# Optimization experiments

Hardware: AMD Instinct MI355X
Metric: run time of the kernel (lower is better)

## Reference

```python
import jax, jax.numpy as jnp
import numpy as np

N = 100000   # nodes
C = 128      # in_channels
K = 32       # n_super_nodes
B = 64       # graphs (num segments)


def setup_inputs() -> dict:
    key = jax.random.key(0)
    k_x, k_b, k_w1, k_b1, k_w2, k_b2 = jax.random.split(key, 6)
    x = jax.random.normal(k_x, (N, C), dtype=jnp.float32)
    batch = jnp.sort(jax.random.randint(k_b, (N,), 0, B))
    # assign_mlp params: Linear(C,C) -> ReLU -> Linear(C,K); stored as [in,out]
    W1 = jax.random.normal(k_w1, (C, C), dtype=jnp.float32) / np.sqrt(C)
    b1 = jax.random.normal(k_b1, (C,), dtype=jnp.float32) * 0.01
    W2 = jax.random.normal(k_w2, (C, K), dtype=jnp.float32) / np.sqrt(C)
    b2 = jax.random.normal(k_b2, (K,), dtype=jnp.float32) * 0.01
    return {"x": x, "batch": batch, "W1": W1, "b1": b1, "W2": W2, "b2": b2}


def reference(x, batch, W1, b1, W2, b2):
    # assignment logits: MLP over node features
    h = jax.nn.relu(x @ W1 + b1)          # [N, C]
    s = jax.nn.softmax(h @ W2 + b2, axis=-1)  # [N, K]
    # outer product per node, then scatter-sum by graph id
    x_expanded = x[:, None, :] * s[:, :, None]  # [N, K, C]
    out = jax.ops.segment_sum(x_expanded, batch, num_segments=B)  # [B, K, C]
    return (out, s)
```

## Files before the change

### kernel.cpp

```cpp
#include <hip/hip_runtime.h>
#include <hip/hip_bf16.h>

#define NN 100000
#define CC 128
#define KK 32
#define BB 64

typedef __bf16 bf16x8 __attribute__((ext_vector_type(8)));
typedef float  f32x4  __attribute__((ext_vector_type(4)));

__device__ __forceinline__ unsigned short f2bf(float v) {
    union { float f; unsigned u; } a; a.f = v;
    unsigned r = a.u + 0x7FFF + ((a.u >> 16) & 1);
    return (unsigned short)(r >> 16);
}
__device__ __forceinline__ float bf2f(unsigned short h) {
    union { unsigned u; float f; } a; a.u = ((unsigned)h) << 16;
    return a.f;
}
__device__ __forceinline__ void unpack_hilo(uint4 a, uint4 b,
                                            bf16x8& hi8, bf16x8& lo8) {
    union { uint4 v[2]; unsigned short s[16]; } U;
    U.v[0] = a; U.v[1] = b;
    union { unsigned short s[8]; bf16x8 v; } H, L;
    #pragma unroll
    for (int j = 0; j < 8; ++j) { H.s[j] = U.s[2 * j]; L.s[j] = U.s[2 * j + 1]; }
    hi8 = H.v; lo8 = L.v;
}

__global__ __launch_bounds__(256) void hp_prep(const int* __restrict__ batch,
                                               const float* __restrict__ W1,
                                               const float* __restrict__ W2,
                                               int* __restrict__ bounds,
                                               unsigned short* __restrict__ w1f,
                                               unsigned short* __restrict__ w2f) {
    if (blockIdx.x == 0 && threadIdx.x <= BB) {
        const int b = threadIdx.x;
        int lo = 0, hi = NN;
        while (lo < hi) {
            const int mid = (lo + hi) >> 1;
            if (batch[mid] < b) lo = mid + 1; else hi = mid;
        }
        bounds[b] = lo;
    }
    const int t = blockIdx.x * 256 + threadIdx.x;
    for (int idx = t; idx < 16384; idx += 2048) {
        const int j    = idx & 7;
        const int lane = (idx >> 3) & 63;
        const int nt   = (idx >> 9) & 7;
        const int kt   = idx >> 12;
        const int k = kt * 32 + (lane >> 4) * 8 + j;
        const int n = nt * 16 + (lane & 15);
        const float w = W1[k * CC + n];
        const unsigned short h = f2bf(w);
        w1f[idx]         = h;
        w1f[16384 + idx] = f2bf(w - bf2f(h));
    }
    for (int idx = t; idx < 4096; idx += 2048) {
        const int j    = idx & 7;
        const int lane = (idx >> 3) & 63;
        const int nt   = (idx >> 9) & 1;
        const int kt   = idx >> 10;
        const int k = kt * 32 + (lane >> 4) * 8 + j;
        const int n = nt * 16 + (lane & 15);
        const float w = W2[k * KK + n];
        const unsigned short h = f2bf(w);
        w2f[idx]        = h;
        w2f[4096 + idx] = f2bf(w - bf2f(h));
    }
}

__global__ __launch_bounds__(256, 6) void hp_mlp(
    const float* __restrict__ x,
    const unsigned short* __restrict__ w1f,
    const unsigned short* __restrict__ w2f,
    const float* __restrict__ b1,
    const float* __restrict__ b2,
    float* __restrict__ s_out)
{
    __shared__ __align__(16) char uni[16896];
    __shared__ float lgT[32][36];
    __shared__ float redm[4][32];
    __shared__ float reds[4][32];

    unsigned short* xa   = (unsigned short*)uni;
    unsigned int*   hs16 = (unsigned int*)uni;

    const int t    = threadIdx.x;
    const int wave = __builtin_amdgcn_readfirstlane(t >> 6);
    const int lane = t & 63;
    const int base = blockIdx.x * 32;

    #pragma unroll
    for (int mt = 0; mt < 2; ++mt) {
        const int q  = mt * 4 + wave;
        const int n  = base + mt * 16 + (lane & 15);
        const int ck = wave * 32 + (lane >> 4) * 8;
        const float4 va = *(const float4*)(x + (size_t)n * CC + ck);
        const float4 vb = *(const float4*)(x + (size_t)n * CC + ck + 4);
        const float v[8] = {va.x, va.y, va.z, va.w, vb.x, vb.y, vb.z, vb.w};
        unsigned short hi[8], lo[8];
        #pragma unroll
        for (int j = 0; j < 8; ++j) {
            hi[j] = f2bf(v[j]);
            lo[j] = f2bf(v[j] - bf2f(hi[j]));
        }
        unsigned short* d0 = xa + (q * 64 + lane) * 8;
        unsigned short* d1 = d0 + 4096;
        *(ushort4*)(d0)     = make_ushort4(hi[0], hi[1], hi[2], hi[3]);
        *(ushort4*)(d0 + 4) = make_ushort4(hi[4], hi[5], hi[6], hi[7]);
        *(ushort4*)(d1)     = make_ushort4(lo[0], lo[1], lo[2], lo[3]);
        *(ushort4*)(d1 + 4) = make_ushort4(lo[4], lo[5], lo[6], lo[7]);
    }
    __syncthreads();

    f32x4 acc[2][2];
    #pragma unroll
    for (int mt = 0; mt < 2; ++mt)
        #pragma unroll
        for (int nl = 0; nl < 2; ++nl)
            acc[mt][nl] = (f32x4){0.f, 0.f, 0.f, 0.f};

    #pragma unroll
    for (int kt = 0; kt < 4; ++kt) {
        bf16x8 ah[2], al[2];
        #pragma unroll
        for (int mt = 0; mt < 2; ++mt) {
            ah[mt] = *(const bf16x8*)(xa + ((mt * 4 + kt) * 64 + lane) * 8);
            al[mt] = *(const bf16x8*)(xa + 4096 + ((mt * 4 + kt) * 64 + lane) * 8);
        }
        #pragma unroll
        for (int nl = 0; nl < 2; ++nl) {
            const int nt = 2 * wave + nl;
            const bf16x8 wh = *(const bf16x8*)(w1f + ((kt * 8 + nt) * 64 + lane) * 8);
            const bf16x8 wl = *(const bf16x8*)(w1f + 16384 + ((kt * 8 + nt) * 64 + lane) * 8);
            #pragma unroll
            for (int mt = 0; mt < 2; ++mt) {
                acc[mt][nl] = __builtin_amdgcn_mfma_f32_16x16x32_bf16(ah[mt], wh, acc[mt][nl], 0, 0, 0);
                acc[mt][nl] = __builtin_amdgcn_mfma_f32_16x16x32_bf16(al[mt], wh, acc[mt][nl], 0, 0, 0);
                acc[mt][nl] = __builtin_amdgcn_mfma_f32_16x16x32_bf16(ah[mt], wl, acc[mt][nl], 0, 0, 0);
            }
        }
    }
    __syncthreads();

    #pragma unroll
    for (int nl = 0; nl < 2; ++nl) {
        const int c = (2 * wave + nl) * 16 + (lane & 15);
        const float bv = b1[c];
        #pragma unroll
        for (int mt = 0; mt < 2; ++mt)
            #pragma unroll
            for (int r = 0; r < 4; ++r) {
                const int node = mt * 16 + (lane >> 4) * 4 + r;
                const float h = fmaxf(acc[mt][nl][r] + bv, 0.f);
                const unsigned short hi = f2bf(h);
                const unsigned short lo = f2bf(h - bf2f(hi));
                hs16[node * 132 + c] = (unsigned)hi | ((unsigned)lo << 16);
            }
    }
    __syncthreads();

    {
        const int mt2 = wave & 1, nt2 = wave >> 1;
        f32x4 dacc = (f32x4){0.f, 0.f, 0.f, 0.f};
        #pragma unroll
        for (int kt = 0; kt < 4; ++kt) {
            const unsigned* hp = hs16 + (mt2 * 16 + (lane & 15)) * 132
                                      + kt * 32 + (lane >> 4) * 8;
            const uint4 u0 = *(const uint4*)hp;
            const uint4 u1 = *(const uint4*)(hp + 4);
            bf16x8 ah, al;
            unpack_hilo(u0, u1, ah, al);
            const bf16x8 wh = *(const bf16x8*)(w2f + ((kt * 2 + nt2) * 64 + lane) * 8);
            const bf16x8 wl = *(const bf16x8*)(w2f + 4096 + ((kt * 2 + nt2) * 64 + lane) * 8);
            dacc = __builtin_amdgcn_mfma_f32_16x16x32_bf16(ah, wh, dacc, 0, 0, 0);
            dacc = __builtin_amdgcn_mfma_f32_16x16x32_bf16(al, wh, dacc, 0, 0, 0);
            dacc = __builtin_amdgcn_mfma_f32_16x16x32_bf16(ah, wl, dacc, 0, 0, 0);
        }
        const int kcol = nt2 * 16 + (lane & 15);
        #pragma unroll
        for (int r = 0; r < 4; ++r) {
            const int node = mt2 * 16 + (lane >> 4) * 4 + r;
            lgT[node][kcol] = dacc[r];
        }
    }
    __syncthreads();

    const int node = lane & 31;
    const int koff = ((lane >> 5) << 4) + wave * 4;
    const float4 bv2 = *(const float4*)(b2 + koff);
    const float4 lv  = *(const float4*)&lgT[node][koff];
    float lg[4] = {lv.x + bv2.x, lv.y + bv2.y, lv.z + bv2.z, lv.w + bv2.w};

    float m = fmaxf(fmaxf(lg[0], lg[1]), fmaxf(lg[2], lg[3]));
    m = fmaxf(m, __shfl_xor(m, 32));
    if (lane < 32) redm[wave][lane] = m;
    __syncthreads();
    const float M = fmaxf(fmaxf(redm[0][node], redm[1][node]),
                          fmaxf(redm[2][node], redm[3][node]));
    const float e0 = __expf(lg[0] - M);
    const float e1 = __expf(lg[1] - M);
    const float e2 = __expf(lg[2] - M);
    const float e3 = __expf(lg[3] - M);
    float sp = (e0 + e1) + (e2 + e3);
    sp += __shfl_xor(sp, 32);
    if (lane < 32) reds[wave][lane] = sp;
    __syncthreads();
    const float S = (reds[0][node] + reds[1][node]) + (reds[2][node] + reds[3][node]);
    const float inv = 1.f / S;
    *(float4*)(s_out + (size_t)(base + node) * KK + koff) =
        make_float4(e0 * inv, e1 * inv, e2 * inv, e3 * inv);
}

__global__ __launch_bounds__(256, 8) void hp_pool(
    const float* __restrict__ x,
    const float* __restrict__ s,
    const int* __restrict__ bounds,
    float* __restrict__ part,
    int nslices)
{
    __shared__ float xs[8][CC];
    __shared__ float ss[8][36];

    const int b = blockIdx.x / nslices;
    const int p = blockIdx.x - b * nslices;
    const int t = threadIdx.x;

    const int gs  = bounds[b];
    const int cnt = bounds[b + 1] - gs;
    const int n0  = gs + (int)(((long long)cnt * p) / nslices);
    const int n1  = gs + (int)(((long long)cnt * (p + 1)) / nslices);

    const int k0 = (t >> 5) * 4;
    const int c0 = (t & 31) * 4;

    float a4[4][4] = {{0.f}};

    for (int nb = n0; nb < n1; nb += 8) {
        const int m = min(8, n1 - nb);
        __syncthreads();
        {
            const int r = t >> 5, cf = t & 31;
            if (r < m)
                *(float4*)&xs[r][cf * 4] = ((const float4*)x)[(size_t)(nb + r) * 32 + cf];
            if (t < 64) {
                const int r2 = t >> 3, kf = t & 7;
                if (r2 < m)
                    *(float4*)&ss[r2][kf * 4] = ((const float4*)s)[(size_t)(nb + r2) * 8 + kf];
            }
        }
        __syncthreads();

        for (int i = 0; i < m; ++i) {
            const float4 xv = *(const float4*)&xs[i][c0];
            const float4 sv = *(const float4*)&ss[i][k0];
            a4[0][0] = fmaf(sv.x, xv.x, a4[0][0]); a4[0][1] = fmaf(sv.x, xv.y, a4[0][1]);
            a4[0][2] = fmaf(sv.x, xv.z, a4[0][2]); a4[0][3] = fmaf(sv.x, xv.w, a4[0][3]);
            a4[1][0] = fmaf(sv.y, xv.x, a4[1][0]); a4[1][1] = fmaf(sv.y, xv.y, a4[1][1]);
            a4[1][2] = fmaf(sv.y, xv.z, a4[1][2]); a4[1][3] = fmaf(sv.y, xv.w, a4[1][3]);
            a4[2][0] = fmaf(sv.z, xv.x, a4[2][0]); a4[2][1] = fmaf(sv.z, xv.y, a4[2][1]);
            a4[2][2] = fmaf(sv.z, xv.z, a4[2][2]); a4[2][3] = fmaf(sv.z, xv.w, a4[2][3]);
            a4[3][0] = fmaf(sv.w, xv.x, a4[3][0]); a4[3][1] = fmaf(sv.w, xv.y, a4[3][1]);
            a4[3][2] = fmaf(sv.w, xv.z, a4[3][2]); a4[3][3] = fmaf(sv.w, xv.w, a4[3][3]);
        }
    }

    float* op = part + (size_t)blockIdx.x * KK * CC;
    #pragma unroll
    for (int a = 0; a < 4; ++a)
        *(float4*)&op[(k0 + a) * CC + c0] =
            make_float4(a4[a][0], a4[a][1], a4[a][2], a4[a][3]);
}

__global__ __launch_bounds__(256) void hp_reduce(const float* __restrict__ part,
                                                 float* __restrict__ out,
                                                 int nslices) {
    const int i = (blockIdx.x * 256 + threadIdx.x) * 4;
    if (i < BB * KK * CC) {
        const int b = i >> 12;
        const int j = i & 4095;
        const float* pp = part + (size_t)b * nslices * 4096 + j;
        float4 r = make_float4(0.f, 0.f, 0.f, 0.f);
        for (int q = 0; q < nslices; ++q) {
            const float4 v = *(const float4*)(pp + (size_t)q * 4096);
            r.x += v.x; r.y += v.y; r.z += v.z; r.w += v.w;
        }
        *(float4*)(out + i) = r;
    }
}

extern "C" void kernel_launch(void* const* d_in, const int* in_sizes, int n_in,
                              void* d_out, int out_size, void* d_ws, size_t ws_size,
                              hipStream_t stream) {
    const float* x     = (const float*)d_in[0];
    const int*   batch = (const int*)d_in[1];
    const float* W1    = (const float*)d_in[2];
    const float* b1    = (const float*)d_in[3];
    const float* W2    = (const float*)d_in[4];
    const float* b2    = (const float*)d_in[5];

    float* out = (float*)d_out;
    float* s   = out + (size_t)BB * KK * CC;

    int*            bounds = (int*)d_ws;
    unsigned short* w1f    = (unsigned short*)((char*)d_ws + 1024);
    unsigned short* w2f    = (unsigned short*)((char*)d_ws + 66560);
    float*          part   = (float*)((char*)d_ws + 82944);

    int nslices = 32;
    while (nslices > 8 &&
           ws_size < 82944 + (size_t)BB * nslices * KK * CC * 4)
        nslices >>= 1;

    hp_prep<<<8, 256, 0, stream>>>(batch, W1, W2, bounds, w1f, w2f);
    hp_mlp<<<NN / 32, 256, 0, stream>>>(x, w1f, w2f, b1, b2, s);
    hp_pool<<<BB * nslices, 256, 0, stream>>>(x, s, bounds, part, nslices);
    hp_reduce<<<BB * KK * CC / (256 * 4), 256, 0, stream>>>(part, out, nslices);
}
```

Before: 152.1 us.

## Pool with bf16 MFMA on pre-swizzled x and s tiles emitted by MLP kernel

```diff
diff --git a/kernel.cpp b/kernel.cpp
--- a/kernel.cpp
+++ b/kernel.cpp
@@ -5,6 +5,7 @@
 #define CC 128
 #define KK 32
 #define BB 64
+#define PS 16
 
 typedef __bf16 bf16x8 __attribute__((ext_vector_type(8)));
 typedef float  f32x4  __attribute__((ext_vector_type(4)));
@@ -76,7 +77,9 @@
     const unsigned short* __restrict__ w2f,
     const float* __restrict__ b1,
     const float* __restrict__ b2,
-    float* __restrict__ s_out)
+    float* __restrict__ s_out,
+    unsigned short* __restrict__ xb,
+    unsigned short* __restrict__ sb)
 {
     __shared__ __align__(16) char uni[16896];
     __shared__ float lgT[32][36];
@@ -111,6 +114,20 @@
         *(ushort4*)(d0 + 4) = make_ushort4(hi[4], hi[5], hi[6], hi[7]);
         *(ushort4*)(d1)     = make_ushort4(lo[0], lo[1], lo[2], lo[3]);
         *(ushort4*)(d1 + 4) = make_ushort4(lo[4], lo[5], lo[6], lo[7]);
+    }
+
+    #pragma unroll
+    for (int cc = 0; cc < 2; ++cc) {
+        const int ct = wave * 2 + cc;
+        const int c  = ct * 16 + (lane & 15);
+        const int nb = base + (lane >> 4) * 8;
+        unsigned short hb[8];
+        #pragma unroll
+        for (int j = 0; j < 8; ++j)
+            hb[j] = f2bf(x[(size_t)(nb + j) * CC + c]);
+        unsigned short* dp = xb + ((size_t)(blockIdx.x * 8 + ct) * 64 + lane) * 8;
+        *(ushort4*)(dp)     = make_ushort4(hb[0], hb[1], hb[2], hb[3]);
+        *(ushort4*)(dp + 4) = make_ushort4(hb[4], hb[5], hb[6], hb[7]);
     }
     __syncthreads();
 
@@ -209,80 +226,88 @@
     __syncthreads();
     const float S = (reds[0][node] + reds[1][node]) + (reds[2][node] + reds[3][node]);
     const float inv = 1.f / S;
-    *(float4*)(s_out + (size_t)(base + node) * KK + koff) =
-        make_float4(e0 * inv, e1 * inv, e2 * inv, e3 * inv);
-}
-
-__global__ __launch_bounds__(256, 8) void hp_pool(
-    const float* __restrict__ x,
-    const float* __restrict__ s,
+    const float4 s4 = make_float4(e0 * inv, e1 * inv, e2 * inv, e3 * inv);
+    *(float4*)(s_out + (size_t)(base + node) * KK + koff) = s4;
+    *(float4*)&lgT[node][koff] = s4;
+    __syncthreads();
+
+    if (wave < 2) {
+        const int k  = wave * 16 + (lane & 15);
+        const int r0 = (lane >> 4) * 8;
+        unsigned short v[8];
+        #pragma unroll
+        for (int j = 0; j < 8; ++j)
+            v[j] = f2bf(lgT[r0 + j][k]);
+        unsigned short* dp = sb + ((size_t)(blockIdx.x * 2 + wave) * 64 + lane) * 8;
+        *(ushort4*)(dp)     = make_ushort4(v[0], v[1], v[2], v[3]);
+        *(ushort4*)(dp + 4) = make_ushort4(v[4], v[5], v[6], v[7]);
+    }
+}
+
+__global__ __launch_bounds__(256) void hp_pool(
+    const unsigned short* __restrict__ xb,
+    const unsigned short* __restrict__ sb,
     const int* __restrict__ bounds,
-    float* __restrict__ part,
-    int nslices)
+    float* __restrict__ part)
 {
-    __shared__ float xs[8][CC];
-    __shared__ float ss[8][36];
-
-    const int b = blockIdx.x / nslices;
-    const int p = blockIdx.x - b * nslices;
-    const int t = threadIdx.x;
-
-    const int gs  = bounds[b];
-    const int cnt = bounds[b + 1] - gs;
-    const int n0  = gs + (int)(((long long)cnt * p) / nslices);
-    const int n1  = gs + (int)(((long long)cnt * (p + 1)) / nslices);
-
-    const int k0 = (t >> 5) * 4;
-    const int c0 = (t & 31) * 4;
-
-    float a4[4][4] = {{0.f}};
-
-    for (int nb = n0; nb < n1; nb += 8) {
-        const int m = min(8, n1 - nb);
-        __syncthreads();
-        {
-            const int r = t >> 5, cf = t & 31;
-            if (r < m)
-                *(float4*)&xs[r][cf * 4] = ((const float4*)x)[(size_t)(nb + r) * 32 + cf];
-            if (t < 64) {
-                const int r2 = t >> 3, kf = t & 7;
-                if (r2 < m)
-                    *(float4*)&ss[r2][kf * 4] = ((const float4*)s)[(size_t)(nb + r2) * 8 + kf];
-            }
-        }
-        __syncthreads();
-
-        for (int i = 0; i < m; ++i) {
-            const float4 xv = *(const float4*)&xs[i][c0];
-            const float4 sv = *(const float4*)&ss[i][k0];
-            a4[0][0] = fmaf(sv.x, xv.x, a4[0][0]); a4[0][1] = fmaf(sv.x, xv.y, a4[0][1]);
-            a4[0][2] = fmaf(sv.x, xv.z, a4[0][2]); a4[0][3] = fmaf(sv.x, xv.w, a4[0][3]);
-            a4[1][0] = fmaf(sv.y, xv.x, a4[1][0]); a4[1][1] = fmaf(sv.y, xv.y, a4[1][1]);
-            a4[1][2] = fmaf(sv.y, xv.z, a4[1][2]); a4[1][3] = fmaf(sv.y, xv.w, a4[1][3]);
-            a4[2][0] = fmaf(sv.z, xv.x, a4[2][0]); a4[2][1] = fmaf(sv.z, xv.y, a4[2][1]);
-            a4[2][2] = fmaf(sv.z, xv.z, a4[2][2]); a4[2][3] = fmaf(sv.z, xv.w, a4[2][3]);
-            a4[3][0] = fmaf(sv.w, xv.x, a4[3][0]); a4[3][1] = fmaf(sv.w, xv.y, a4[3][1]);
-            a4[3][2] = fmaf(sv.w, xv.z, a4[3][2]); a4[3][3] = fmaf(sv.w, xv.w, a4[3][3]);
+    const int b = blockIdx.x / PS;
+    const int p = blockIdx.x - b * PS;
+    const int wave = __builtin_amdgcn_readfirstlane(threadIdx.x >> 6);
+    const int lane = threadIdx.x & 63;
+
+    const int gs = bounds[b], ge = bounds[b + 1];
+    const int c0g = gs >> 5;
+    const int cnt = ((ge + 31) >> 5) - c0g;
+    const int ch0 = c0g + (cnt * p) / PS;
+    const int ch1 = c0g + (cnt * (p + 1)) / PS;
+
+    const int mt    = wave & 1;
+    const int chalf = wave >> 1;
+    const int nrow  = (lane >> 4) * 8;
+
+    f32x4 acc[4];
+    #pragma unroll
+    for (int i = 0; i < 4; ++i) acc[i] = (f32x4){0.f, 0.f, 0.f, 0.f};
+
+    for (int ch = ch0; ch < ch1; ++ch) {
+        union { ushort4 u[2]; unsigned short s[8]; bf16x8 v; } A;
+        const unsigned short* ap = sb + ((size_t)(ch * 2 + mt) * 64 + lane) * 8;
+        A.u[0] = *(const ushort4*)ap;
+        A.u[1] = *(const ushort4*)(ap + 4);
+        const int nb = ch * 32 + nrow;
+        #pragma unroll
+        for (int j = 0; j < 8; ++j)
+            if (nb + j < gs || nb + j >= ge) A.s[j] = 0;
+        #pragma unroll
+        for (int i = 0; i < 4; ++i) {
+            const int ct = chalf * 4 + i;
+            const bf16x8 Bv = *(const bf16x8*)(xb + ((size_t)(ch * 8 + ct) * 64 + lane) * 8);
+            acc[i] = __builtin_amdgcn_mfma_f32_16x16x32_bf16(A.v, Bv, acc[i], 0, 0, 0);
         }
     }
 
     float* op = part + (size_t)blockIdx.x * KK * CC;
     #pragma unroll
-    for (int a = 0; a < 4; ++a)
-        *(float4*)&op[(k0 + a) * CC + c0] =
-            make_float4(a4[a][0], a4[a][1], a4[a][2], a4[a][3]);
+    for (int i = 0; i < 4; ++i) {
+        const int c = (chalf * 4 + i) * 16 + (lane & 15);
+        #pragma unroll
+        for (int r = 0; r < 4; ++r) {
+            const int k = mt * 16 + (lane >> 4) * 4 + r;
+            op[k * CC + c] = acc[i][r];
+        }
+    }
 }
 
 __global__ __launch_bounds__(256) void hp_reduce(const float* __restrict__ part,
-                                                 float* __restrict__ out,
-                                                 int nslices) {
+                                                 float* __restrict__ out) {
     const int i = (blockIdx.x * 256 + threadIdx.x) * 4;
     if (i < BB * KK * CC) {
         const int b = i >> 12;
         const int j = i & 4095;
-        const float* pp = part + (size_t)b * nslices * 4096 + j;
+        const float* pp = part + (size_t)b * PS * 4096 + j;
         float4 r = make_float4(0.f, 0.f, 0.f, 0.f);
-        for (int q = 0; q < nslices; ++q) {
+        #pragma unroll 4
+        for (int q = 0; q < PS; ++q) {
             const float4 v = *(const float4*)(pp + (size_t)q * 4096);
             r.x += v.x; r.y += v.y; r.z += v.z; r.w += v.w;
         }
@@ -303,18 +328,16 @@
     float* out = (float*)d_out;
     float* s   = out + (size_t)BB * KK * CC;
 
-    int*            bounds = (int*)d_ws;
-    unsigned short* w1f    = (unsigned short*)((char*)d_ws + 1024);
-    unsigned short* w2f    = (unsigned short*)((char*)d_ws + 66560);
-    float*          part   = (float*)((char*)d_ws + 82944);
-
-    int nslices = 32;
-    while (nslices > 8 &&
-           ws_size < 82944 + (size_t)BB * nslices * KK * CC * 4)
-        nslices >>= 1;
+    char* ws = (char*)d_ws;
+    int*            bounds = (int*)ws;
+    unsigned short* w1f    = (unsigned short*)(ws + 1024);
+    unsigned short* w2f    = (unsigned short*)(ws + 66560);
+    unsigned short* xb     = (unsigned short*)(ws + 82944);
+    unsigned short* sb     = (unsigned short*)(ws + 82944 + 25600000);
+    float*          part   = (float*)(ws + 82944 + 25600000 + 6400000);
 
     hp_prep<<<8, 256, 0, stream>>>(batch, W1, W2, bounds, w1f, w2f);
-    hp_mlp<<<NN / 32, 256, 0, stream>>>(x, w1f, w2f, b1, b2, s);
-    hp_pool<<<BB * nslices, 256, 0, stream>>>(x, s, bounds, part, nslices);
-    hp_reduce<<<BB * KK * CC / (256 * 4), 256, 0, stream>>>(part, out, nslices);
-}
+    hp_mlp<<<NN / 32, 256, 0, stream>>>(x, w1f, w2f, b1, b2, s, xb, sb);
+    hp_pool<<<BB * PS, 256, 0, stream>>>(xb, sb, bounds, part);
+    hp_reduce<<<BB * KK * CC / (256 * 4), 256, 0, stream>>>(part, out);
+}
```

Result: faster. 135.4 us (-11.0%).
